# Optimization experiments

Measured on AMD Instinct MI355X. Metric: run time of the kernel, lower is better.

Reference implementation:

```python
import jax, jax.numpy as jnp
import numpy as np

B, S, H, E = 2, 2048, 16, 64
INV_SCALE = 8.0  # sqrt(head_dim); forward divides scores by this


def setup_inputs() -> dict:
    key = jax.random.key(0)
    ks = jax.random.split(key, 10)
    return {
        "query": jax.random.normal(ks[0], (B, S, H, E), dtype=jnp.float32),
        "key": jax.random.normal(ks[1], (B, S, H, E), dtype=jnp.float32),
        "value": jax.random.normal(ks[2], (B, S, H, E), dtype=jnp.float32),
        "attn_mask": jax.random.randint(ks[3], (B, S), 0, 2, dtype=jnp.int32),
        "Wq": jax.random.normal(ks[4], (E, E), dtype=jnp.float32) / np.sqrt(E),
        "bq": jax.random.normal(ks[5], (E,), dtype=jnp.float32) * 0.02,
        "Wk": jax.random.normal(ks[6], (E, E), dtype=jnp.float32) / np.sqrt(E),
        "bk": jax.random.normal(ks[7], (E,), dtype=jnp.float32) * 0.02,
        "Wv": jax.random.normal(ks[8], (E, E), dtype=jnp.float32) / np.sqrt(E),
        "bv": jax.random.normal(ks[9], (E,), dtype=jnp.float32) * 0.02,
    }


def reference(query, key, value, attn_mask, Wq, bq, Wk, bk, Wv, bv):
    # Linear projections over the last (embed) dim; torch Linear: x @ W.T + b
    q = jnp.einsum('bshe,fe->bhsf', query, Wq) + bq  # [B,H,S,E] (permute 0,2,1,3 fused)
    k = jnp.einsum('bshe,fe->bhsf', key, Wk) + bk
    v = jnp.einsum('bshe,fe->bhsf', value, Wv) + bv
    scores = jnp.einsum('bhqe,bhke->bhqk', q, k) / INV_SCALE  # [B,H,S,S]
    # mask: positions where attn_mask == 0 get -inf, broadcast over (1,1,k_len)
    masked = attn_mask[:, None, None, :] == 0  # [B,1,1,S]
    scores = jnp.where(masked, -jnp.inf, scores)
    attn = jax.nn.softmax(scores, axis=-1)
    out = jnp.einsum('bhqk,bhke->bqhe', attn, v)  # permute back to [B,S,H,E]
    return out
```

## Files before the change

### kernel.cpp

```cpp
#include <hip/hip_runtime.h>


#define BATCH 2
#define SEQ   2048
#define NH    16
#define DE    64
#define LDOF  68
#define NKT   (SEQ / 64)
#define LOG2E 1.44269504088896340736f
#define CSHIFT 16.0f

using bf16x8   = __attribute__((ext_vector_type(8))) __bf16;
using bf16x4   = __attribute__((ext_vector_type(4))) __bf16;
using bf16x2   = __attribute__((ext_vector_type(2))) __bf16;
using floatx2  = __attribute__((ext_vector_type(2))) float;
using floatx4  = __attribute__((ext_vector_type(4))) float;
using floatx16 = __attribute__((ext_vector_type(16))) float;
using ushortx4 = __attribute__((ext_vector_type(4))) unsigned short;
using ushortx8 = __attribute__((ext_vector_type(8))) unsigned short;
using uintx4   = __attribute__((ext_vector_type(4))) unsigned int;

__device__ __forceinline__ ushortx4 cvt4(floatx4 f) {
    bf16x4 h = __builtin_convertvector(f, bf16x4);
    return __builtin_bit_cast(ushortx4, h);
}

__device__ __forceinline__ unsigned int pkbf16(float a, float b) {
    floatx2 f = {a, b};
    return __builtin_bit_cast(unsigned int, __builtin_convertvector(f, bf16x2));
}

__device__ __forceinline__ void pl32swap(unsigned int& x, unsigned int& y) {
    __asm__ volatile("v_permlane32_swap_b32 %0, %1" : "+v"(x), "+v"(y));
}

__device__ __forceinline__ void glds16(const unsigned short* g, unsigned short* l) {
    __builtin_amdgcn_global_load_lds(
        (const __attribute__((address_space(1))) unsigned int*)g,
        (__attribute__((address_space(3))) unsigned int*)l, 16, 0, 0);
}

__global__ __launch_bounds__(256) void proj_kernel(
    const float* __restrict__ xq, const float* __restrict__ xk, const float* __restrict__ xv,
    const float* __restrict__ Wq, const float* __restrict__ bq,
    const float* __restrict__ Wk, const float* __restrict__ bk,
    const float* __restrict__ Wv, const float* __restrict__ bv,
    unsigned short* __restrict__ qb, unsigned short* __restrict__ kb,
    unsigned short* __restrict__ vtb)
{
    __shared__ __align__(16) unsigned short Wb[64 * 72];
    __shared__ __align__(16) unsigned short Xb[8 * 1160];
    __shared__ __align__(16) unsigned short Ob[12288];
    __shared__ float blds[64];

    const int t  = threadIdx.x;
    const int bi = blockIdx.x;
    const int hh = bi & 1;
    const int st = (bi >> 1) & 127;
    const int b  = (bi >> 8) & 1;
    const int p  = bi >> 9;
    const int h0 = hh * 8;
    const int lane = t & 63, w = t >> 6, quad = lane >> 4, l16 = lane & 15;

    const float* x    = (p == 0) ? xq : (p == 1) ? xk : xv;
    const float* W    = (p == 0) ? Wq : (p == 1) ? Wk : Wv;
    const float* bias = (p == 0) ? bq : (p == 1) ? bk : bv;

    #pragma unroll
    for (int i = 0; i < 8; ++i) {
        int idx = i * 256 + t;
        int s = idx >> 7, rem = idx & 127, h = rem >> 4, e4 = (rem & 15) * 4;
        floatx4 xv4 = *(const floatx4*)(x + ((size_t)(b * SEQ + st * 16 + s) * NH + h0 + h) * DE + e4);
        *(ushortx4*)&Xb[h * 1160 + s * 72 + e4] = cvt4(xv4);
    }
    #pragma unroll
    for (int i = 0; i < 4; ++i) {
        int idx = i * 256 + t;
        int row = idx >> 4, c4 = (idx & 15) * 4;
        floatx4 wv4 = *(const floatx4*)(W + row * 64 + c4);
        *(ushortx4*)&Wb[row * 72 + c4] = cvt4(wv4);
    }
    if (t < 64) blds[t] = bias[t];
    __syncthreads();

    if (p < 2) {
        bf16x8 a0 = *(const bf16x8*)&Wb[(w * 16 + l16) * 72 + quad * 8];
        bf16x8 a1 = *(const bf16x8*)&Wb[(w * 16 + l16) * 72 + 32 + quad * 8];
        floatx4 bf4 = *(const floatx4*)&blds[w * 16 + quad * 4];
        const float scale = (p == 0) ? 0.125f * LOG2E : 1.0f;
        #pragma unroll
        for (int h = 0; h < 8; ++h) {
            bf16x8 b0 = *(const bf16x8*)&Xb[h * 1160 + l16 * 72 + quad * 8];
            bf16x8 b1 = *(const bf16x8*)&Xb[h * 1160 + l16 * 72 + 32 + quad * 8];
            floatx4 c = {0.f, 0.f, 0.f, 0.f};
            c = __builtin_amdgcn_mfma_f32_16x16x32_bf16(a0, b0, c, 0, 0, 0);
            c = __builtin_amdgcn_mfma_f32_16x16x32_bf16(a1, b1, c, 0, 0, 0);
            floatx4 v;
            v[0] = (c[0] + bf4[0]) * scale; v[1] = (c[1] + bf4[1]) * scale;
            v[2] = (c[2] + bf4[2]) * scale; v[3] = (c[3] + bf4[3]) * scale;
            *(ushortx4*)&Ob[h * 1160 + l16 * 72 + w * 16 + quad * 4] = cvt4(v);
        }
    } else {
        bf16x8 b0 = *(const bf16x8*)&Wb[(w * 16 + l16) * 72 + quad * 8];
        bf16x8 b1 = *(const bf16x8*)&Wb[(w * 16 + l16) * 72 + 32 + quad * 8];
        const float bw = blds[w * 16 + l16];
        #pragma unroll
        for (int h = 0; h < 8; ++h) {
            bf16x8 a0 = *(const bf16x8*)&Xb[h * 1160 + l16 * 72 + quad * 8];
            bf16x8 a1 = *(const bf16x8*)&Xb[h * 1160 + l16 * 72 + 32 + quad * 8];
            floatx4 c = {0.f, 0.f, 0.f, 0.f};
            c = __builtin_amdgcn_mfma_f32_16x16x32_bf16(a0, b0, c, 0, 0, 0);
            c = __builtin_amdgcn_mfma_f32_16x16x32_bf16(a1, b1, c, 0, 0, 0);
            floatx4 v;
            v[0] = c[0] + bw; v[1] = c[1] + bw; v[2] = c[2] + bw; v[3] = c[3] + bw;
            *(ushortx4*)&Ob[h * 1536 + (w * 16 + l16) * 24 + quad * 4] = cvt4(v);
        }
    }
    __syncthreads();

    if (p < 2) {
        unsigned short* dst = (p == 0) ? qb : kb;
        #pragma unroll
        for (int i = 0; i < 4; ++i) {
            int idx = i * 256 + t;
            int c = idx & 7, s = (idx >> 3) & 15, h = idx >> 7;
            ushortx8 v = *(const ushortx8*)&Ob[h * 1160 + s * 72 + c * 8];
            *(ushortx8*)(dst + ((size_t)(b * 16 + h0 + h) * SEQ + st * 16 + s) * 64
                         + ((c ^ (s & 7)) * 8)) = v;
        }
    } else {
        #pragma unroll
        for (int i = 0; i < 4; ++i) {
            int idx = i * 256 + t;
            int cl = idx & 1, e = (idx >> 1) & 63, h = idx >> 7;
            ushortx8 v = *(const ushortx8*)&Ob[h * 1536 + e * 24 + cl * 8];
            int c = (st & 3) * 2 + cl;
            *(ushortx8*)(vtb + ((size_t)(b * 16 + h0 + h) * 64 + e) * SEQ
                         + (st >> 2) * 64 + ((c ^ (e & 7)) * 8)) = v;
        }
    }
}

__global__ __launch_bounds__(512, 4) void attn_kernel(
    const unsigned short* __restrict__ qb, const unsigned short* __restrict__ kb,
    const unsigned short* __restrict__ vtb, const int* __restrict__ mask,
    float* __restrict__ out)
{
    __shared__ __align__(16) char smem[16384 + 16384 + 16384 + 512];
    unsigned short* Kl = (unsigned short*)smem;
    unsigned short* Vl = (unsigned short*)(smem + 16384);
    unsigned short* Pq = (unsigned short*)(smem + 32768);
    float*          Ml = (float*)(smem + 49152);
    float*          Ol = (float*)smem;
    float*          Ll = (float*)(smem + 34816);

    const int t  = threadIdx.x;
    const int qt = blockIdx.x, bh = blockIdx.y;
    const int b  = bh >> 4, h = bh & 15;
    const int q0 = qt * 128;
    const int lane = t & 63, w = t >> 6;
    const int hi = lane >> 5, l31 = lane & 31;
    const int qw = w & 3, kblk = w >> 2;
    const int sw7 = l31 & 7;

    const unsigned short* kbase = kb + (size_t)bh * SEQ * DE;
    const unsigned short* vbase = vtb + (size_t)bh * DE * SEQ;
    const unsigned short* qsrc  = qb + ((size_t)bh * SEQ + q0) * DE;
    const int* mrow = mask + b * SEQ;

    glds16(qsrc + (w * 16) * DE + lane * 8,      Pq + (w * 16) * 64);
    glds16(qsrc + (w * 16 + 8) * DE + lane * 8,  Pq + (w * 16 + 8) * 64);
    glds16(kbase + (size_t)(w * 8) * DE + lane * 8, Kl + w * 512);
    glds16(vbase + (size_t)(w * 8 + (lane >> 3)) * SEQ + (lane & 7) * 8, Vl + w * 512);
    if (t < 64) Ml[t] = mrow[t] ? -CSHIFT : -1e30f;
    int mreg = (t < 64) ? mrow[64 + t] : 0;
    __syncthreads();

    bf16x8 qf[4];
    #pragma unroll
    for (int ks = 0; ks < 4; ++ks)
        qf[ks] = *(const bf16x8*)&Pq[(qw * 32 + l31) * 64 + (((ks * 2 + hi) ^ sw7) * 8)];

    floatx16 o0, o1;
    #pragma unroll
    for (int i = 0; i < 16; ++i) { o0[i] = 0.f; o1[i] = 0.f; }
    float lp = 0.f;

    for (int kt = 0; kt < NKT; ++kt) {
        const int cur = kt & 1, nxt = cur ^ 1;
        const unsigned short* Kc = Kl + cur * 4096;
        const unsigned short* Vc = Vl + cur * 4096;
        const float*          Mc = Ml + cur * 64;

        if (kt + 1 < NKT) {
            const int k1 = (kt + 1) * 64;
            glds16(kbase + (size_t)(k1 + w * 8) * DE + lane * 8, Kl + nxt * 4096 + w * 512);
            glds16(vbase + (size_t)(w * 8 + (lane >> 3)) * SEQ + k1 + (lane & 7) * 8,
                   Vl + nxt * 4096 + w * 512);
            if (t < 64) Ml[nxt * 64 + t] = mreg ? -CSHIFT : -1e30f;
            mreg = (t < 64 && kt + 2 < NKT) ? mrow[(kt + 2) * 64 + t] : 0;
        }

        floatx16 sc;
        #pragma unroll
        for (int g = 0; g < 4; ++g) {
            floatx4 mb = *(const floatx4*)&Mc[kblk * 32 + g * 8 + hi * 4];
            sc[4 * g + 0] = mb[0]; sc[4 * g + 1] = mb[1];
            sc[4 * g + 2] = mb[2]; sc[4 * g + 3] = mb[3];
        }
        #pragma unroll
        for (int ks = 0; ks < 4; ++ks) {
            bf16x8 kf = *(const bf16x8*)&Kc[(kblk * 32 + l31) * 64 + (((ks * 2 + hi) ^ sw7) * 8)];
            sc = __builtin_amdgcn_mfma_f32_32x32x16_bf16(kf, qf[ks], sc, 0, 0, 0);
        }

        #pragma unroll
        for (int r = 0; r < 16; ++r)
            sc[r] = __builtin_amdgcn_exp2f(sc[r]);
        {
            float a0 = sc[0] + sc[1],   a1 = sc[2] + sc[3];
            float a2 = sc[4] + sc[5],   a3 = sc[6] + sc[7];
            float a4 = sc[8] + sc[9],   a5 = sc[10] + sc[11];
            float a6 = sc[12] + sc[13], a7 = sc[14] + sc[15];
            lp += ((a0 + a1) + (a2 + a3)) + ((a4 + a5) + (a6 + a7));
        }

        unsigned int wd0 = pkbf16(sc[0], sc[1]),   wd1 = pkbf16(sc[2], sc[3]);
        unsigned int wd2 = pkbf16(sc[4], sc[5]),   wd3 = pkbf16(sc[6], sc[7]);
        unsigned int wd4 = pkbf16(sc[8], sc[9]),   wd5 = pkbf16(sc[10], sc[11]);
        unsigned int wd6 = pkbf16(sc[12], sc[13]), wd7 = pkbf16(sc[14], sc[15]);
        pl32swap(wd0, wd2); pl32swap(wd1, wd3);
        pl32swap(wd4, wd6); pl32swap(wd5, wd7);
        uintx4 f0v = {wd0, wd1, wd2, wd3};
        uintx4 f1v = {wd4, wd5, wd6, wd7};
        bf16x8 pf0 = __builtin_bit_cast(bf16x8, f0v);
        bf16x8 pf1 = __builtin_bit_cast(bf16x8, f1v);

        #pragma unroll
        for (int s = 0; s < 2; ++s) {
            const bf16x8 pf = s ? pf1 : pf0;
            const int cc = ((kblk * 4 + s * 2 + hi) ^ sw7) * 8;
            bf16x8 v0 = *(const bf16x8*)&Vc[l31 * 64 + cc];
            bf16x8 v1 = *(const bf16x8*)&Vc[(32 + l31) * 64 + cc];
            o0 = __builtin_amdgcn_mfma_f32_32x32x16_bf16(v0, pf, o0, 0, 0, 0);
            o1 = __builtin_amdgcn_mfma_f32_32x32x16_bf16(v1, pf, o1, 0, 0, 0);
        }

        __syncthreads();
    }

    const int qrow = qw * 32 + l31;
    Ll[qrow * 4 + kblk * 2 + hi] = lp;
    if (kblk == 1) {
        #pragma unroll
        for (int g = 0; g < 4; ++g) {
            floatx4 t0 = {o0[4*g+0], o0[4*g+1], o0[4*g+2], o0[4*g+3]};
            *(floatx4*)&Ol[qrow * LDOF + g * 8 + hi * 4] = t0;
            floatx4 t1 = {o1[4*g+0], o1[4*g+1], o1[4*g+2], o1[4*g+3]};
            *(floatx4*)&Ol[qrow * LDOF + 32 + g * 8 + hi * 4] = t1;
        }
    }
    __syncthreads();
    if (kblk == 0) {
        floatx4 lv = *(const floatx4*)&Ll[qrow * 4];
        float invl = __builtin_amdgcn_rcpf(lv[0] + lv[1] + lv[2] + lv[3]);
        #pragma unroll
        for (int g = 0; g < 4; ++g) {
            floatx4 t0 = *(floatx4*)&Ol[qrow * LDOF + g * 8 + hi * 4];
            t0[0] = (t0[0] + o0[4*g+0]) * invl; t0[1] = (t0[1] + o0[4*g+1]) * invl;
            t0[2] = (t0[2] + o0[4*g+2]) * invl; t0[3] = (t0[3] + o0[4*g+3]) * invl;
            *(floatx4*)&Ol[qrow * LDOF + g * 8 + hi * 4] = t0;
            floatx4 t1 = *(floatx4*)&Ol[qrow * LDOF + 32 + g * 8 + hi * 4];
            t1[0] = (t1[0] + o1[4*g+0]) * invl; t1[1] = (t1[1] + o1[4*g+1]) * invl;
            t1[2] = (t1[2] + o1[4*g+2]) * invl; t1[3] = (t1[3] + o1[4*g+3]) * invl;
            *(floatx4*)&Ol[qrow * LDOF + 32 + g * 8 + hi * 4] = t1;
        }
    }
    __syncthreads();
    {
        const int quad = lane >> 4, l16 = lane & 15;
        #pragma unroll
        for (int pass = 0; pass < 4; ++pass) {
            int rl  = w * 16 + pass * 4 + quad;
            int col = l16 * 4;
            floatx4 tv = *(const floatx4*)&Ol[rl * LDOF + col];
            *(floatx4*)(out + (((size_t)b * SEQ + q0 + rl) * NH + h) * DE + col) = tv;
        }
    }
}

extern "C" void kernel_launch(void* const* d_in, const int* in_sizes, int n_in,
                              void* d_out, int out_size, void* d_ws, size_t ws_size,
                              hipStream_t stream) {
    const float* query = (const float*)d_in[0];
    const float* key   = (const float*)d_in[1];
    const float* value = (const float*)d_in[2];
    const int*   mask  = (const int*)d_in[3];
    const float* Wq = (const float*)d_in[4];
    const float* bq = (const float*)d_in[5];
    const float* Wk = (const float*)d_in[6];
    const float* bk = (const float*)d_in[7];
    const float* Wv = (const float*)d_in[8];
    const float* bv = (const float*)d_in[9];

    const size_t tensor_elems = (size_t)BATCH * NH * SEQ * DE;
    unsigned short* qb  = (unsigned short*)d_ws;
    unsigned short* kb  = qb + tensor_elems;
    unsigned short* vtb = kb + tensor_elems;

    proj_kernel<<<dim3(3 * BATCH * 128 * 2), 256, 0, stream>>>(
        query, key, value, Wq, bq, Wk, bk, Wv, bv, qb, kb, vtb);
    attn_kernel<<<dim3(SEQ / 128, BATCH * NH), 512, 0, stream>>>(
        qb, kb, vtb, mask, (float*)d_out);
}
```

Measured before the change: 152.2 us.

## Pre-swizzle Q/K/V into MFMA fragment order and load directly from global

The projection kernel now writes Q, K and V^T in a layout that already matches the per-lane MFMA operand order. The attention kernel can then read K and V fragments straight from global memory (through cache) instead of staging them through double-buffered LDS, which also removes the per-tile __syncthreads. The whole mask row is converted into LDS once up front, and the grid is flattened with a remapping that groups the 8 heads sharing data onto neighbouring workgroups for cache locality. The cost is that each wave re-reads K/V from L2, since the LDS sharing across the 4 query waves is gone, and global load latency is now exposed in the loop without explicit prefetch.

```diff
diff --git a/kernel.cpp b/kernel.cpp
--- a/kernel.cpp
+++ b/kernel.cpp
@@ -19,6 +19,7 @@
 using ushortx4 = __attribute__((ext_vector_type(4))) unsigned short;
 using ushortx8 = __attribute__((ext_vector_type(8))) unsigned short;
 using uintx4   = __attribute__((ext_vector_type(4))) unsigned int;
+using intx4    = __attribute__((ext_vector_type(4))) int;
 
 __device__ __forceinline__ ushortx4 cvt4(floatx4 f) {
     bf16x4 h = __builtin_convertvector(f, bf16x4);
@@ -32,12 +33,6 @@
 
 __device__ __forceinline__ void pl32swap(unsigned int& x, unsigned int& y) {
     __asm__ volatile("v_permlane32_swap_b32 %0, %1" : "+v"(x), "+v"(y));
-}
-
-__device__ __forceinline__ void glds16(const unsigned short* g, unsigned short* l) {
-    __builtin_amdgcn_global_load_lds(
-        (const __attribute__((address_space(1))) unsigned int*)g,
-        (__attribute__((address_space(3))) unsigned int*)l, 16, 0, 0);
 }
 
 __global__ __launch_bounds__(256) void proj_kernel(
@@ -120,23 +115,26 @@
 
     if (p < 2) {
         unsigned short* dst = (p == 0) ? qb : kb;
+        const int rb  = st >> 1;
+        const int sl0 = (st & 1) * 16;
         #pragma unroll
         for (int i = 0; i < 4; ++i) {
             int idx = i * 256 + t;
-            int c = idx & 7, s = (idx >> 3) & 15, h = idx >> 7;
-            ushortx8 v = *(const ushortx8*)&Ob[h * 1160 + s * 72 + c * 8];
-            *(ushortx8*)(dst + ((size_t)(b * 16 + h0 + h) * SEQ + st * 16 + s) * 64
-                         + ((c ^ (s & 7)) * 8)) = v;
+            int j = idx & 7, s = (idx >> 3) & 15, h = idx >> 7;
+            ushortx8 v = *(const ushortx8*)&Ob[h * 1160 + s * 72 + j * 8];
+            size_t off = ((size_t)((b * 16 + h0 + h) * 64) + rb) * 2048 + j * 256 + (sl0 + s) * 8;
+            *(ushortx8*)(dst + off) = v;
         }
     } else {
+        const int kt  = st >> 2;
+        const int cb  = (st & 3) * 2;
         #pragma unroll
         for (int i = 0; i < 4; ++i) {
             int idx = i * 256 + t;
             int cl = idx & 1, e = (idx >> 1) & 63, h = idx >> 7;
             ushortx8 v = *(const ushortx8*)&Ob[h * 1536 + e * 24 + cl * 8];
-            int c = (st & 3) * 2 + cl;
-            *(ushortx8*)(vtb + ((size_t)(b * 16 + h0 + h) * 64 + e) * SEQ
-                         + (st >> 2) * 64 + ((c ^ (e & 7)) * 8)) = v;
+            size_t off = (((size_t)(b * 16 + h0 + h) * 32 + kt) * 8 + cb + cl) * 512 + e * 8;
+            *(ushortx8*)(vtb + off) = v;
         }
     }
 }
@@ -146,40 +144,40 @@
     const unsigned short* __restrict__ vtb, const int* __restrict__ mask,
     float* __restrict__ out)
 {
-    __shared__ __align__(16) char smem[16384 + 16384 + 16384 + 512];
-    unsigned short* Kl = (unsigned short*)smem;
-    unsigned short* Vl = (unsigned short*)(smem + 16384);
-    unsigned short* Pq = (unsigned short*)(smem + 32768);
-    float*          Ml = (float*)(smem + 49152);
-    float*          Ol = (float*)smem;
-    float*          Ll = (float*)(smem + 34816);
-
-    const int t  = threadIdx.x;
-    const int qt = blockIdx.x, bh = blockIdx.y;
-    const int b  = bh >> 4, h = bh & 15;
-    const int q0 = qt * 128;
+    __shared__ __align__(16) char smem[36864 + 8192];
+    float* Ol = (float*)smem;
+    float* Ll = (float*)(smem + 34816);
+    float* Ml = (float*)(smem + 36864);
+
+    const int wg  = blockIdx.x;
+    const int bh  = ((wg >> 3) >> 4) * 8 + (wg & 7);
+    const int qt  = (wg >> 3) & 15;
+    const int b   = bh >> 4, h = bh & 15;
+    const int q0  = qt * 128;
+    const int t   = threadIdx.x;
     const int lane = t & 63, w = t >> 6;
     const int hi = lane >> 5, l31 = lane & 31;
     const int qw = w & 3, kblk = w >> 2;
-    const int sw7 = l31 & 7;
-
-    const unsigned short* kbase = kb + (size_t)bh * SEQ * DE;
-    const unsigned short* vbase = vtb + (size_t)bh * DE * SEQ;
-    const unsigned short* qsrc  = qb + ((size_t)bh * SEQ + q0) * DE;
-    const int* mrow = mask + b * SEQ;
-
-    glds16(qsrc + (w * 16) * DE + lane * 8,      Pq + (w * 16) * 64);
-    glds16(qsrc + (w * 16 + 8) * DE + lane * 8,  Pq + (w * 16 + 8) * 64);
-    glds16(kbase + (size_t)(w * 8) * DE + lane * 8, Kl + w * 512);
-    glds16(vbase + (size_t)(w * 8 + (lane >> 3)) * SEQ + (lane & 7) * 8, Vl + w * 512);
-    if (t < 64) Ml[t] = mrow[t] ? -CSHIFT : -1e30f;
-    int mreg = (t < 64) ? mrow[64 + t] : 0;
-    __syncthreads();
-
+
+    {
+        intx4 mv = *(const intx4*)(mask + b * SEQ + t * 4);
+        Ml[t * 4 + 0] = mv[0] ? -CSHIFT : -1e30f;
+        Ml[t * 4 + 1] = mv[1] ? -CSHIFT : -1e30f;
+        Ml[t * 4 + 2] = mv[2] ? -CSHIFT : -1e30f;
+        Ml[t * 4 + 3] = mv[3] ? -CSHIFT : -1e30f;
+    }
+
+    const unsigned short* qp = qb + ((size_t)(bh * 64 + qt * 4 + qw)) * 2048 + hi * 256 + l31 * 8;
     bf16x8 qf[4];
     #pragma unroll
     for (int ks = 0; ks < 4; ++ks)
-        qf[ks] = *(const bf16x8*)&Pq[(qw * 32 + l31) * 64 + (((ks * 2 + hi) ^ sw7) * 8)];
+        qf[ks] = *(const bf16x8*)(qp + ks * 512);
+
+    const unsigned short* kp = kb + ((size_t)(bh * 64 + kblk)) * 2048 + hi * 256 + l31 * 8;
+    const unsigned short* vp = vtb + (size_t)bh * 131072 + (kblk * 4 + hi) * 512 + l31 * 8;
+    const float* Mb = Ml + kblk * 32 + hi * 4;
+
+    __syncthreads();
 
     floatx16 o0, o1;
     #pragma unroll
@@ -187,32 +185,30 @@
     float lp = 0.f;
 
     for (int kt = 0; kt < NKT; ++kt) {
-        const int cur = kt & 1, nxt = cur ^ 1;
-        const unsigned short* Kc = Kl + cur * 4096;
-        const unsigned short* Vc = Vl + cur * 4096;
-        const float*          Mc = Ml + cur * 64;
-
-        if (kt + 1 < NKT) {
-            const int k1 = (kt + 1) * 64;
-            glds16(kbase + (size_t)(k1 + w * 8) * DE + lane * 8, Kl + nxt * 4096 + w * 512);
-            glds16(vbase + (size_t)(w * 8 + (lane >> 3)) * SEQ + k1 + (lane & 7) * 8,
-                   Vl + nxt * 4096 + w * 512);
-            if (t < 64) Ml[nxt * 64 + t] = mreg ? -CSHIFT : -1e30f;
-            mreg = (t < 64 && kt + 2 < NKT) ? mrow[(kt + 2) * 64 + t] : 0;
-        }
-
+        const unsigned short* kq = kp + kt * 4096;
+        bf16x8 kf0 = *(const bf16x8*)(kq);
+        bf16x8 kf1 = *(const bf16x8*)(kq + 512);
+        bf16x8 kf2 = *(const bf16x8*)(kq + 1024);
+        bf16x8 kf3 = *(const bf16x8*)(kq + 1536);
+
+        const float* Mc = Mb + kt * 64;
         floatx16 sc;
         #pragma unroll
         for (int g = 0; g < 4; ++g) {
-            floatx4 mb = *(const floatx4*)&Mc[kblk * 32 + g * 8 + hi * 4];
+            floatx4 mb = *(const floatx4*)(Mc + g * 8);
             sc[4 * g + 0] = mb[0]; sc[4 * g + 1] = mb[1];
             sc[4 * g + 2] = mb[2]; sc[4 * g + 3] = mb[3];
         }
-        #pragma unroll
-        for (int ks = 0; ks < 4; ++ks) {
-            bf16x8 kf = *(const bf16x8*)&Kc[(kblk * 32 + l31) * 64 + (((ks * 2 + hi) ^ sw7) * 8)];
-            sc = __builtin_amdgcn_mfma_f32_32x32x16_bf16(kf, qf[ks], sc, 0, 0, 0);
-        }
+        sc = __builtin_amdgcn_mfma_f32_32x32x16_bf16(kf0, qf[0], sc, 0, 0, 0);
+        sc = __builtin_amdgcn_mfma_f32_32x32x16_bf16(kf1, qf[1], sc, 0, 0, 0);
+        sc = __builtin_amdgcn_mfma_f32_32x32x16_bf16(kf2, qf[2], sc, 0, 0, 0);
+        sc = __builtin_amdgcn_mfma_f32_32x32x16_bf16(kf3, qf[3], sc, 0, 0, 0);
+
+        const unsigned short* vq = vp + kt * 4096;
+        bf16x8 vf00 = *(const bf16x8*)(vq);
+        bf16x8 vf01 = *(const bf16x8*)(vq + 256);
+        bf16x8 vf10 = *(const bf16x8*)(vq + 1024);
+        bf16x8 vf11 = *(const bf16x8*)(vq + 1280);
 
         #pragma unroll
         for (int r = 0; r < 16; ++r)
@@ -236,17 +232,10 @@
         bf16x8 pf0 = __builtin_bit_cast(bf16x8, f0v);
         bf16x8 pf1 = __builtin_bit_cast(bf16x8, f1v);
 
-        #pragma unroll
-        for (int s = 0; s < 2; ++s) {
-            const bf16x8 pf = s ? pf1 : pf0;
-            const int cc = ((kblk * 4 + s * 2 + hi) ^ sw7) * 8;
-            bf16x8 v0 = *(const bf16x8*)&Vc[l31 * 64 + cc];
-            bf16x8 v1 = *(const bf16x8*)&Vc[(32 + l31) * 64 + cc];
-            o0 = __builtin_amdgcn_mfma_f32_32x32x16_bf16(v0, pf, o0, 0, 0, 0);
-            o1 = __builtin_amdgcn_mfma_f32_32x32x16_bf16(v1, pf, o1, 0, 0, 0);
-        }
-
-        __syncthreads();
+        o0 = __builtin_amdgcn_mfma_f32_32x32x16_bf16(vf00, pf0, o0, 0, 0, 0);
+        o1 = __builtin_amdgcn_mfma_f32_32x32x16_bf16(vf01, pf0, o1, 0, 0, 0);
+        o0 = __builtin_amdgcn_mfma_f32_32x32x16_bf16(vf10, pf1, o0, 0, 0, 0);
+        o1 = __builtin_amdgcn_mfma_f32_32x32x16_bf16(vf11, pf1, o1, 0, 0, 0);
     }
 
     const int qrow = qw * 32 + l31;
@@ -310,6 +299,6 @@
 
     proj_kernel<<<dim3(3 * BATCH * 128 * 2), 256, 0, stream>>>(
         query, key, value, Wq, bq, Wk, bk, Wv, bv, qb, kb, vtb);
-    attn_kernel<<<dim3(SEQ / 128, BATCH * NH), 512, 0, stream>>>(
+    attn_kernel<<<dim3(512), 512, 0, stream>>>(
         qb, kb, vtb, mask, (float*)d_out);
 }
```

Result: no change. 152.0 us (-0.1%).
